# Performance work log

Hardware: AMD Instinct MI355X
Metric: run time of the kernel (lower is better)

Reference implementation:

```python
import jax, jax.numpy as jnp
import numpy as np
import math

MAX_REL_POS = 32  # max_relative_position

def _sincos_table(d_model, max_len):
    pos = np.arange(max_len)[:, None].astype(np.float32)
    div = np.exp(np.arange(0, d_model, 2).astype(np.float32) * (-math.log(10000.0) / d_model))
    pe = np.zeros((max_len, d_model), dtype=np.float32)
    pe[:, 0::2] = np.sin(pos * div)
    pe[:, 1::2] = np.cos(pos * div)
    return jnp.asarray(pe)

def setup_inputs() -> dict:
    rng = jax.random.key(0)
    k1, k2, k3 = jax.random.split(rng, 3)
    B, H, S, D = 4, 16, 1024, 64
    pe = _sincos_table(D, 2 * MAX_REL_POS + 1)  # fixed (non-trainable) buffer
    return {
        "query": jax.random.normal(k1, (B, H, S, D), jnp.float32),
        "key": jax.random.normal(k2, (B, H, S, D), jnp.float32),
        "value": jax.random.normal(k3, (B, H, S, D), jnp.float32),
        "pe_k": pe,
        "pe_v": pe,
    }

def reference(query, key, value, pe_k, pe_v):
    B, H, S, D = query.shape
    # relative distance indices: clip(k - q, -P, P) + P  -> [S, S]
    dist = jnp.clip(jnp.arange(S)[None, :] - jnp.arange(S)[:, None],
                    -MAX_REL_POS, MAX_REL_POS) + MAX_REL_POS
    R_k = pe_k[dist]  # [S, S, D]
    R_v = pe_v[dist]  # [S, S, D]
    scores = jnp.einsum('bhqd,bhkd->bhqk', query, key)
    scores = scores + jnp.einsum('bhqd,qkd->bhqk', query, R_k)
    scores = scores / math.sqrt(D)
    # one_direction=True -> causal mask
    causal = jnp.tril(jnp.ones((S, S), dtype=bool))
    scores = jnp.where(causal[None, None], scores, jnp.float32(-1e9))
    p_attn = jax.nn.softmax(scores, axis=-1)
    output = jnp.einsum('bhqk,bhkd->bhqd', p_attn, value)
    output = output + jnp.einsum('bhqv,qvd->bhqd', p_attn, R_v)
    return output, p_attn
```

## Files before the change

kernel.cpp:

```cpp
#include <hip/hip_runtime.h>

typedef __attribute__((ext_vector_type(8))) short bfrag;
typedef __attribute__((ext_vector_type(4))) float ffrag;

namespace {
constexpr int Sc = 1024, Dc = 64;
constexpr int P2 = 72;
constexpr float SCALE = 0.125f;
}

__device__ __forceinline__ unsigned short f2bf(float f) {
    unsigned u = __builtin_bit_cast(unsigned, f);
    u += 0x7fffu + ((u >> 16) & 1u);
    return (unsigned short)(u >> 16);
}
__device__ __forceinline__ bfrag pack8(float4 a, float4 b) {
    bfrag r;
    r[0] = (short)f2bf(a.x); r[1] = (short)f2bf(a.y);
    r[2] = (short)f2bf(a.z); r[3] = (short)f2bf(a.w);
    r[4] = (short)f2bf(b.x); r[5] = (short)f2bf(b.y);
    r[6] = (short)f2bf(b.z); r[7] = (short)f2bf(b.w);
    return r;
}
#define MFMA(a, b, c) __builtin_amdgcn_mfma_f32_16x16x32_bf16((a), (b), (c), 0, 0, 0)

__global__ __launch_bounds__(256, 3)
void relattn(const float* __restrict__ Qg, const float* __restrict__ Kg,
             const float* __restrict__ Vg, const float* __restrict__ pek,
             const float* __restrict__ pev, float* __restrict__ outg,
             float* __restrict__ pbuf)
{
    __shared__ __align__(16) char smem[53760];
    unsigned short* Qs = (unsigned short*)smem;
    unsigned short* Ks = (unsigned short*)(smem + 9216);
    unsigned short* Vt = (unsigned short*)(smem + 18432);
    unsigned short* Pt = (unsigned short*)(smem + 27648);
    float* Ts = (float*)(smem + 36864);
    float* Ws = (float*)(smem + 45312);
    float* W0 = (float*)(smem + 53504);
    float* Ot = (float*)(smem + 9216);

    const int tid  = threadIdx.x;
    const int bh   = blockIdx.y;
    const int wv   = tid >> 6;
    const int lane = tid & 63;
    const int n    = lane & 15;
    const int quad = lane >> 4;

    const float* Qbh = Qg + (size_t)bh * Sc * Dc;
    const float* Kbh = Kg + (size_t)bh * Sc * Dc;
    const float* Vbh = Vg + (size_t)bh * Sc * Dc;
    float* pbh = pbuf + (size_t)bh * Sc * Sc;
    float* obh = outg + (size_t)bh * Sc * Dc;

    const int sr  = tid >> 2;
    const int sc  = (tid & 3) * 16;
    const int kp  = tid & 31;
    const int vd0 = (tid >> 5) * 8;

    for (int half = 0; half < 2; ++half) {
        const int qt = half ? (15 - (int)blockIdx.x) : (int)blockIdx.x;
        const int qrow = wv * 16 + quad * 4;

        __syncthreads();

        {
            const float* src = Qbh + (size_t)(qt * 64 + sr) * Dc + sc;
            float4 a = *(const float4*)(src);
            float4 b = *(const float4*)(src + 4);
            float4 c = *(const float4*)(src + 8);
            float4 d = *(const float4*)(src + 12);
            *(bfrag*)&Qs[sr * P2 + sc]     = pack8(a, b);
            *(bfrag*)&Qs[sr * P2 + sc + 8] = pack8(c, d);
        }
        for (int idx = tid; idx < 64 * 32; idx += 256) Ws[idx] = 0.f;
        for (int i = tid; i < 135; i += 256) {
            bfrag z = {};
            *(bfrag*)&Ks[33 * P2 + i * 8] = z;
        }
        if (tid < 132) {
            int r = tid >> 2, c0 = (tid & 3) * 16;
            const float* src = pek + (size_t)r * Dc + c0;
            float4 a = *(const float4*)(src);
            float4 b = *(const float4*)(src + 4);
            float4 c = *(const float4*)(src + 8);
            float4 d = *(const float4*)(src + 12);
            *(bfrag*)&Ks[r * P2 + c0]     = pack8(a, b);
            *(bfrag*)&Ks[r * P2 + c0 + 8] = pack8(c, d);
        }
        __syncthreads();

        bfrag qa0 = *(bfrag*)&Qs[(wv * 16 + n) * P2 + quad * 8];
        bfrag qa1 = *(bfrag*)&Qs[(wv * 16 + n) * P2 + 32 + quad * 8];

        #pragma unroll
        for (int sub = 0; sub < 3; ++sub) {
            bfrag b0 = *(bfrag*)&Ks[(sub * 16 + n) * P2 + quad * 8];
            bfrag b1 = *(bfrag*)&Ks[(sub * 16 + n) * P2 + 32 + quad * 8];
            ffrag c = {};
            c = MFMA(qa0, b0, c);
            c = MFMA(qa1, b1, c);
            int j = sub * 16 + n;
            if (j <= 32) {
                #pragma unroll
                for (int reg = 0; reg < 4; ++reg)
                    Ts[(qrow + reg) * 33 + j] = c[reg];
            }
        }
        __syncthreads();

        float ts0[4];
        #pragma unroll
        for (int reg = 0; reg < 4; ++reg) ts0[reg] = Ts[(qrow + reg) * 33];

        {
            const int zb = (qt + 1) * 64;
            if (zb < Sc) {
                const int z4 = (Sc - zb) >> 2;
                const float4 z = make_float4(0.f, 0.f, 0.f, 0.f);
                for (int r = 0; r < 64; ++r) {
                    float4* rp = (float4*)(pbh + (size_t)(qt * 64 + r) * Sc + zb);
                    for (int c4 = tid; c4 < z4; c4 += 256) rp[c4] = z;
                }
            }
        }

        float lsum[4] = {0.f, 0.f, 0.f, 0.f};
        for (int kt = 0; kt <= qt; ++kt) {
            const bool bnd = (kt >= qt - 1);
            const float* ksrc = Kbh + (size_t)(kt * 64 + sr) * Dc + sc;
            float4 ka = *(const float4*)(ksrc);
            float4 kb = *(const float4*)(ksrc + 4);
            float4 kc = *(const float4*)(ksrc + 8);
            float4 kd = *(const float4*)(ksrc + 12);
            __syncthreads();
            *(bfrag*)&Ks[sr * P2 + sc]     = pack8(ka, kb);
            *(bfrag*)&Ks[sr * P2 + sc + 8] = pack8(kc, kd);
            __syncthreads();
            #pragma unroll
            for (int sub = 0; sub < 4; ++sub) {
                bfrag b0 = *(bfrag*)&Ks[(sub * 16 + n) * P2 + quad * 8];
                bfrag b1 = *(bfrag*)&Ks[(sub * 16 + n) * P2 + 32 + quad * 8];
                ffrag c = {};
                c = MFMA(qa0, b0, c);
                c = MFMA(qa1, b1, c);
                const int k = kt * 64 + sub * 16 + n;
                if (!bnd) {
                    #pragma unroll
                    for (int reg = 0; reg < 4; ++reg)
                        lsum[reg] += __expf((c[reg] + ts0[reg]) * SCALE);
                } else {
                    #pragma unroll
                    for (int reg = 0; reg < 4; ++reg) {
                        int jrel = k - (qt * 64 + qrow + reg) + 32;
                        if (jrel <= 32) {
                            int jcl = jrel < 0 ? 0 : jrel;
                            lsum[reg] += __expf((c[reg] + Ts[(qrow + reg) * 33 + jcl]) * SCALE);
                        }
                    }
                }
            }
        }
        float rinv[4];
        #pragma unroll
        for (int reg = 0; reg < 4; ++reg) {
            float l = lsum[reg];
            l += __shfl_xor(l, 1);
            l += __shfl_xor(l, 2);
            l += __shfl_xor(l, 4);
            l += __shfl_xor(l, 8);
            rinv[reg] = 1.f / l;
        }

        ffrag oacc[4];
        #pragma unroll
        for (int i = 0; i < 4; ++i) { ffrag z = {}; oacc[i] = z; }

        for (int kt = 0; kt <= qt; ++kt) {
            const bool bnd = (kt >= qt - 1);
            const float* ksrc = Kbh + (size_t)(kt * 64 + sr) * Dc + sc;
            float4 ka = *(const float4*)(ksrc);
            float4 kb = *(const float4*)(ksrc + 4);
            float4 kc = *(const float4*)(ksrc + 8);
            float4 kd = *(const float4*)(ksrc + 12);
            const float* vsrc = Vbh + (size_t)(kt * 64 + 2 * kp) * Dc + vd0;
            float4 v0a = *(const float4*)(vsrc);
            float4 v0b = *(const float4*)(vsrc + 4);
            float4 v1a = *(const float4*)(vsrc + Dc);
            float4 v1b = *(const float4*)(vsrc + Dc + 4);
            __syncthreads();
            *(bfrag*)&Ks[sr * P2 + sc]     = pack8(ka, kb);
            *(bfrag*)&Ks[sr * P2 + sc + 8] = pack8(kc, kd);
            {
                float r0[8] = {v0a.x, v0a.y, v0a.z, v0a.w, v0b.x, v0b.y, v0b.z, v0b.w};
                float r1[8] = {v1a.x, v1a.y, v1a.z, v1a.w, v1b.x, v1b.y, v1b.z, v1b.w};
                #pragma unroll
                for (int i = 0; i < 8; ++i) {
                    unsigned pk = (unsigned)f2bf(r0[i]) | ((unsigned)f2bf(r1[i]) << 16);
                    *(unsigned*)&Vt[(vd0 + i) * P2 + 2 * kp] = pk;
                }
            }
            __syncthreads();
            #pragma unroll
            for (int sub = 0; sub < 4; ++sub) {
                bfrag b0 = *(bfrag*)&Ks[(sub * 16 + n) * P2 + quad * 8];
                bfrag b1 = *(bfrag*)&Ks[(sub * 16 + n) * P2 + 32 + quad * 8];
                ffrag c = {};
                c = MFMA(qa0, b0, c);
                c = MFMA(qa1, b1, c);
                const int k = kt * 64 + sub * 16 + n;
                float* prow = pbh + (size_t)(qt * 64 + qrow) * Sc + k;
                if (!bnd) {
                    #pragma unroll
                    for (int reg = 0; reg < 4; ++reg) {
                        float p = __expf((c[reg] + ts0[reg]) * SCALE) * rinv[reg];
                        prow[(size_t)reg * Sc] = p;
                        Pt[(qrow + reg) * P2 + sub * 16 + n] = (unsigned short)f2bf(p);
                    }
                } else {
                    #pragma unroll
                    for (int reg = 0; reg < 4; ++reg) {
                        int jrel = k - (qt * 64 + qrow + reg) + 32;
                        float p = 0.f;
                        if (jrel <= 32) {
                            int jcl = jrel < 0 ? 0 : jrel;
                            p = __expf((c[reg] + Ts[(qrow + reg) * 33 + jcl]) * SCALE) * rinv[reg];
                        }
                        prow[(size_t)reg * Sc] = p;
                        Pt[(qrow + reg) * P2 + sub * 16 + n] = (unsigned short)f2bf(p);
                        if ((unsigned)(jrel - 1) < 32u) Ws[(qrow + reg) * 32 + jrel - 1] = p;
                    }
                }
            }
            __syncthreads();
            bfrag pb0 = *(bfrag*)&Pt[(wv * 16 + n) * P2 + quad * 8];
            bfrag pb1 = *(bfrag*)&Pt[(wv * 16 + n) * P2 + 32 + quad * 8];
            #pragma unroll
            for (int ds = 0; ds < 4; ++ds) {
                bfrag va0 = *(bfrag*)&Vt[(ds * 16 + n) * P2 + quad * 8];
                bfrag va1 = *(bfrag*)&Vt[(ds * 16 + n) * P2 + 32 + quad * 8];
                oacc[ds] = MFMA(va0, pb0, oacc[ds]);
                oacc[ds] = MFMA(va1, pb1, oacc[ds]);
            }
        }

        __syncthreads();
        if (tid < 64) {
            float s = 0.f;
            #pragma unroll
            for (int j = 0; j < 32; ++j) s += Ws[tid * 32 + j];
            W0[tid] = 1.f - s;
        }
        {
            int q = tid >> 2, j0 = (tid & 3) * 8;
            #pragma unroll
            for (int i = 0; i < 8; i += 2) {
                unsigned pk = (unsigned)f2bf(Ws[q * 32 + j0 + i]) |
                              ((unsigned)f2bf(Ws[q * 32 + j0 + i + 1]) << 16);
                *(unsigned*)&Pt[q * P2 + j0 + i] = pk;
            }
        }
        {
            int jj = tid >> 3, d0 = (tid & 7) * 8;
            const float* src = pev + (size_t)(jj + 1) * Dc + d0;
            float4 a = *(const float4*)(src);
            float4 b = *(const float4*)(src + 4);
            float vr[8] = {a.x, a.y, a.z, a.w, b.x, b.y, b.z, b.w};
            #pragma unroll
            for (int i = 0; i < 8; ++i)
                Vt[(d0 + i) * P2 + jj] = (unsigned short)f2bf(vr[i]);
        }
        __syncthreads();
        {
            bfrag pb = *(bfrag*)&Pt[(wv * 16 + n) * P2 + quad * 8];
            #pragma unroll
            for (int ds = 0; ds < 4; ++ds) {
                bfrag va = *(bfrag*)&Vt[(ds * 16 + n) * P2 + quad * 8];
                oacc[ds] = MFMA(va, pb, oacc[ds]);
            }
        }
        float w0q = W0[wv * 16 + n];
        __syncthreads();
        #pragma unroll
        for (int ds = 0; ds < 4; ++ds) {
            float4 ov;
            ov.x = oacc[ds][0] + w0q * pev[ds * 16 + quad * 4 + 0];
            ov.y = oacc[ds][1] + w0q * pev[ds * 16 + quad * 4 + 1];
            ov.z = oacc[ds][2] + w0q * pev[ds * 16 + quad * 4 + 2];
            ov.w = oacc[ds][3] + w0q * pev[ds * 16 + quad * 4 + 3];
            *(float4*)&Ot[(wv * 16 + n) * 68 + ds * 16 + quad * 4] = ov;
        }
        __syncthreads();
        {
            int r = tid >> 2, c0 = (tid & 3) * 16;
            float* dst = obh + (size_t)(qt * 64 + r) * Dc + c0;
            *(float4*)(dst)      = *(float4*)&Ot[r * 68 + c0];
            *(float4*)(dst + 4)  = *(float4*)&Ot[r * 68 + c0 + 4];
            *(float4*)(dst + 8)  = *(float4*)&Ot[r * 68 + c0 + 8];
            *(float4*)(dst + 12) = *(float4*)&Ot[r * 68 + c0 + 12];
        }
    }
}

extern "C" void kernel_launch(void* const* d_in, const int* in_sizes, int n_in,
                              void* d_out, int out_size, void* d_ws, size_t ws_size,
                              hipStream_t stream)
{
    const float* Q   = (const float*)d_in[0];
    const float* K   = (const float*)d_in[1];
    const float* V   = (const float*)d_in[2];
    const float* pek = (const float*)d_in[3];
    const float* pev = (const float*)d_in[4];
    float* out  = (float*)d_out;
    float* pbuf = out + (size_t)64 * Sc * Dc;

    dim3 grid(8, 64);
    relattn<<<grid, 256, 0, stream>>>(Q, K, V, pek, pev, out, pbuf);
}
```

Measured before the change: 391.3 us.

## Fuse two-pass softmax into a single pass with double-buffered K/V prefetch

Drops the separate row-sum pass over K. Unnormalized probabilities are written to the P output and fed to the PV MFMA in one sweep, and the 1/sum scaling is applied afterwards to the output accumulator and in a rescale pass over the written P rows. K and V tiles now use double-buffered LDS: the next tile's global loads are issued before the current tile's compute, which removes one sync pair per iteration. Shared memory grows to about 72 KB and the occupancy hint drops from 3 to 2 blocks. The P matrix is read back and rewritten once for normalization, and exp is applied without subtracting a running max.

```diff
diff --git a/kernel.cpp b/kernel.cpp
--- a/kernel.cpp
+++ b/kernel.cpp
@@ -24,20 +24,23 @@
 }
 #define MFMA(a, b, c) __builtin_amdgcn_mfma_f32_16x16x32_bf16((a), (b), (c), 0, 0, 0)
 
-__global__ __launch_bounds__(256, 3)
+__global__ __launch_bounds__(256, 2)
 void relattn(const float* __restrict__ Qg, const float* __restrict__ Kg,
              const float* __restrict__ Vg, const float* __restrict__ pek,
              const float* __restrict__ pev, float* __restrict__ outg,
              float* __restrict__ pbuf)
 {
-    __shared__ __align__(16) char smem[53760];
-    unsigned short* Qs = (unsigned short*)smem;
-    unsigned short* Ks = (unsigned short*)(smem + 9216);
-    unsigned short* Vt = (unsigned short*)(smem + 18432);
-    unsigned short* Pt = (unsigned short*)(smem + 27648);
-    float* Ts = (float*)(smem + 36864);
-    float* Ws = (float*)(smem + 45312);
-    float* W0 = (float*)(smem + 53504);
+    __shared__ __align__(16) char smem[72448];
+    unsigned short* Qs  = (unsigned short*)smem;
+    unsigned short* Ks0 = (unsigned short*)(smem + 9216);
+    unsigned short* Ks1 = (unsigned short*)(smem + 18432);
+    unsigned short* Vt0 = (unsigned short*)(smem + 27648);
+    unsigned short* Vt1 = (unsigned short*)(smem + 36864);
+    unsigned short* Pt  = (unsigned short*)(smem + 46080);
+    float* Ts = (float*)(smem + 55296);
+    float* Ws = (float*)(smem + 63744);
+    float* W0 = (float*)(smem + 71936);
+    float* Rl = (float*)(smem + 72192);
     float* Ot = (float*)(smem + 9216);
 
     const int tid  = threadIdx.x;
@@ -76,7 +79,7 @@
         for (int idx = tid; idx < 64 * 32; idx += 256) Ws[idx] = 0.f;
         for (int i = tid; i < 135; i += 256) {
             bfrag z = {};
-            *(bfrag*)&Ks[33 * P2 + i * 8] = z;
+            *(bfrag*)&Ks0[33 * P2 + i * 8] = z;
         }
         if (tid < 132) {
             int r = tid >> 2, c0 = (tid & 3) * 16;
@@ -85,8 +88,21 @@
             float4 b = *(const float4*)(src + 4);
             float4 c = *(const float4*)(src + 8);
             float4 d = *(const float4*)(src + 12);
-            *(bfrag*)&Ks[r * P2 + c0]     = pack8(a, b);
-            *(bfrag*)&Ks[r * P2 + c0 + 8] = pack8(c, d);
+            *(bfrag*)&Ks0[r * P2 + c0]     = pack8(a, b);
+            *(bfrag*)&Ks0[r * P2 + c0 + 8] = pack8(c, d);
+        }
+        float4 ka, kb, kc, kd, v0a, v0b, v1a, v1b;
+        {
+            const float* ksrc = Kbh + (size_t)sr * Dc + sc;
+            ka = *(const float4*)(ksrc);
+            kb = *(const float4*)(ksrc + 4);
+            kc = *(const float4*)(ksrc + 8);
+            kd = *(const float4*)(ksrc + 12);
+            const float* vsrc = Vbh + (size_t)(2 * kp) * Dc + vd0;
+            v0a = *(const float4*)(vsrc);
+            v0b = *(const float4*)(vsrc + 4);
+            v1a = *(const float4*)(vsrc + Dc);
+            v1b = *(const float4*)(vsrc + Dc + 4);
         }
         __syncthreads();
 
@@ -95,8 +111,8 @@
 
         #pragma unroll
         for (int sub = 0; sub < 3; ++sub) {
-            bfrag b0 = *(bfrag*)&Ks[(sub * 16 + n) * P2 + quad * 8];
-            bfrag b1 = *(bfrag*)&Ks[(sub * 16 + n) * P2 + 32 + quad * 8];
+            bfrag b0 = *(bfrag*)&Ks0[(sub * 16 + n) * P2 + quad * 8];
+            bfrag b1 = *(bfrag*)&Ks0[(sub * 16 + n) * P2 + 32 + quad * 8];
             ffrag c = {};
             c = MFMA(qa0, b0, c);
             c = MFMA(qa1, b1, c);
@@ -113,98 +129,50 @@
         #pragma unroll
         for (int reg = 0; reg < 4; ++reg) ts0[reg] = Ts[(qrow + reg) * 33];
 
-        {
-            const int zb = (qt + 1) * 64;
-            if (zb < Sc) {
-                const int z4 = (Sc - zb) >> 2;
-                const float4 z = make_float4(0.f, 0.f, 0.f, 0.f);
-                for (int r = 0; r < 64; ++r) {
-                    float4* rp = (float4*)(pbh + (size_t)(qt * 64 + r) * Sc + zb);
-                    for (int c4 = tid; c4 < z4; c4 += 256) rp[c4] = z;
-                }
-            }
-        }
+        *(bfrag*)&Ks0[sr * P2 + sc]     = pack8(ka, kb);
+        *(bfrag*)&Ks0[sr * P2 + sc + 8] = pack8(kc, kd);
+        {
+            float r0[8] = {v0a.x, v0a.y, v0a.z, v0a.w, v0b.x, v0b.y, v0b.z, v0b.w};
+            float r1[8] = {v1a.x, v1a.y, v1a.z, v1a.w, v1b.x, v1b.y, v1b.z, v1b.w};
+            #pragma unroll
+            for (int i = 0; i < 8; ++i) {
+                unsigned pk = (unsigned)f2bf(r0[i]) | ((unsigned)f2bf(r1[i]) << 16);
+                *(unsigned*)&Vt0[(vd0 + i) * P2 + 2 * kp] = pk;
+            }
+        }
+        __syncthreads();
 
         float lsum[4] = {0.f, 0.f, 0.f, 0.f};
+        ffrag oacc[4];
+        #pragma unroll
+        for (int i = 0; i < 4; ++i) { ffrag z = {}; oacc[i] = z; }
+
         for (int kt = 0; kt <= qt; ++kt) {
             const bool bnd = (kt >= qt - 1);
-            const float* ksrc = Kbh + (size_t)(kt * 64 + sr) * Dc + sc;
-            float4 ka = *(const float4*)(ksrc);
-            float4 kb = *(const float4*)(ksrc + 4);
-            float4 kc = *(const float4*)(ksrc + 8);
-            float4 kd = *(const float4*)(ksrc + 12);
-            __syncthreads();
-            *(bfrag*)&Ks[sr * P2 + sc]     = pack8(ka, kb);
-            *(bfrag*)&Ks[sr * P2 + sc + 8] = pack8(kc, kd);
-            __syncthreads();
+            const bool pf  = (kt < qt);
+            unsigned short* Kc = (kt & 1) ? Ks1 : Ks0;
+            unsigned short* Vc = (kt & 1) ? Vt1 : Vt0;
+            unsigned short* Kn = (kt & 1) ? Ks0 : Ks1;
+            unsigned short* Vn = (kt & 1) ? Vt0 : Vt1;
+
+            float4 nka, nkb, nkc, nkd, nv0a, nv0b, nv1a, nv1b;
+            if (pf) {
+                const float* ksrc = Kbh + (size_t)((kt + 1) * 64 + sr) * Dc + sc;
+                nka = *(const float4*)(ksrc);
+                nkb = *(const float4*)(ksrc + 4);
+                nkc = *(const float4*)(ksrc + 8);
+                nkd = *(const float4*)(ksrc + 12);
+                const float* vsrc = Vbh + (size_t)((kt + 1) * 64 + 2 * kp) * Dc + vd0;
+                nv0a = *(const float4*)(vsrc);
+                nv0b = *(const float4*)(vsrc + 4);
+                nv1a = *(const float4*)(vsrc + Dc);
+                nv1b = *(const float4*)(vsrc + Dc + 4);
+            }
+
             #pragma unroll
             for (int sub = 0; sub < 4; ++sub) {
-                bfrag b0 = *(bfrag*)&Ks[(sub * 16 + n) * P2 + quad * 8];
-                bfrag b1 = *(bfrag*)&Ks[(sub * 16 + n) * P2 + 32 + quad * 8];
-                ffrag c = {};
-                c = MFMA(qa0, b0, c);
-                c = MFMA(qa1, b1, c);
-                const int k = kt * 64 + sub * 16 + n;
-                if (!bnd) {
-                    #pragma unroll
-                    for (int reg = 0; reg < 4; ++reg)
-                        lsum[reg] += __expf((c[reg] + ts0[reg]) * SCALE);
-                } else {
-                    #pragma unroll
-                    for (int reg = 0; reg < 4; ++reg) {
-                        int jrel = k - (qt * 64 + qrow + reg) + 32;
-                        if (jrel <= 32) {
-                            int jcl = jrel < 0 ? 0 : jrel;
-                            lsum[reg] += __expf((c[reg] + Ts[(qrow + reg) * 33 + jcl]) * SCALE);
-                        }
-                    }
-                }
-            }
-        }
-        float rinv[4];
-        #pragma unroll
-        for (int reg = 0; reg < 4; ++reg) {
-            float l = lsum[reg];
-            l += __shfl_xor(l, 1);
-            l += __shfl_xor(l, 2);
-            l += __shfl_xor(l, 4);
-            l += __shfl_xor(l, 8);
-            rinv[reg] = 1.f / l;
-        }
-
-        ffrag oacc[4];
-        #pragma unroll
-        for (int i = 0; i < 4; ++i) { ffrag z = {}; oacc[i] = z; }
-
-        for (int kt = 0; kt <= qt; ++kt) {
-            const bool bnd = (kt >= qt - 1);
-            const float* ksrc = Kbh + (size_t)(kt * 64 + sr) * Dc + sc;
-            float4 ka = *(const float4*)(ksrc);
-            float4 kb = *(const float4*)(ksrc + 4);
-            float4 kc = *(const float4*)(ksrc + 8);
-            float4 kd = *(const float4*)(ksrc + 12);
-            const float* vsrc = Vbh + (size_t)(kt * 64 + 2 * kp) * Dc + vd0;
-            float4 v0a = *(const float4*)(vsrc);
-            float4 v0b = *(const float4*)(vsrc + 4);
-            float4 v1a = *(const float4*)(vsrc + Dc);
-            float4 v1b = *(const float4*)(vsrc + Dc + 4);
-            __syncthreads();
-            *(bfrag*)&Ks[sr * P2 + sc]     = pack8(ka, kb);
-            *(bfrag*)&Ks[sr * P2 + sc + 8] = pack8(kc, kd);
-            {
-                float r0[8] = {v0a.x, v0a.y, v0a.z, v0a.w, v0b.x, v0b.y, v0b.z, v0b.w};
-                float r1[8] = {v1a.x, v1a.y, v1a.z, v1a.w, v1b.x, v1b.y, v1b.z, v1b.w};
-                #pragma unroll
-                for (int i = 0; i < 8; ++i) {
-                    unsigned pk = (unsigned)f2bf(r0[i]) | ((unsigned)f2bf(r1[i]) << 16);
-                    *(unsigned*)&Vt[(vd0 + i) * P2 + 2 * kp] = pk;
-                }
-            }
-            __syncthreads();
-            #pragma unroll
-            for (int sub = 0; sub < 4; ++sub) {
-                bfrag b0 = *(bfrag*)&Ks[(sub * 16 + n) * P2 + quad * 8];
-                bfrag b1 = *(bfrag*)&Ks[(sub * 16 + n) * P2 + 32 + quad * 8];
+                bfrag b0 = *(bfrag*)&Kc[(sub * 16 + n) * P2 + quad * 8];
+                bfrag b1 = *(bfrag*)&Kc[(sub * 16 + n) * P2 + 32 + quad * 8];
                 ffrag c = {};
                 c = MFMA(qa0, b0, c);
                 c = MFMA(qa1, b1, c);
@@ -213,7 +181,8 @@
                 if (!bnd) {
                     #pragma unroll
                     for (int reg = 0; reg < 4; ++reg) {
-                        float p = __expf((c[reg] + ts0[reg]) * SCALE) * rinv[reg];
+                        float p = __expf((c[reg] + ts0[reg]) * SCALE);
+                        lsum[reg] += p;
                         prow[(size_t)reg * Sc] = p;
                         Pt[(qrow + reg) * P2 + sub * 16 + n] = (unsigned short)f2bf(p);
                     }
@@ -224,7 +193,8 @@
                         float p = 0.f;
                         if (jrel <= 32) {
                             int jcl = jrel < 0 ? 0 : jrel;
-                            p = __expf((c[reg] + Ts[(qrow + reg) * 33 + jcl]) * SCALE) * rinv[reg];
+                            p = __expf((c[reg] + Ts[(qrow + reg) * 33 + jcl]) * SCALE);
+                            lsum[reg] += p;
                         }
                         prow[(size_t)reg * Sc] = p;
                         Pt[(qrow + reg) * P2 + sub * 16 + n] = (unsigned short)f2bf(p);
@@ -232,24 +202,52 @@
                     }
                 }
             }
+            if (pf) {
+                *(bfrag*)&Kn[sr * P2 + sc]     = pack8(nka, nkb);
+                *(bfrag*)&Kn[sr * P2 + sc + 8] = pack8(nkc, nkd);
+                float r0[8] = {nv0a.x, nv0a.y, nv0a.z, nv0a.w, nv0b.x, nv0b.y, nv0b.z, nv0b.w};
+                float r1[8] = {nv1a.x, nv1a.y, nv1a.z, nv1a.w, nv1b.x, nv1b.y, nv1b.z, nv1b.w};
+                #pragma unroll
+                for (int i = 0; i < 8; ++i) {
+                    unsigned pk = (unsigned)f2bf(r0[i]) | ((unsigned)f2bf(r1[i]) << 16);
+                    *(unsigned*)&Vn[(vd0 + i) * P2 + 2 * kp] = pk;
+                }
+            }
             __syncthreads();
+
             bfrag pb0 = *(bfrag*)&Pt[(wv * 16 + n) * P2 + quad * 8];
             bfrag pb1 = *(bfrag*)&Pt[(wv * 16 + n) * P2 + 32 + quad * 8];
             #pragma unroll
             for (int ds = 0; ds < 4; ++ds) {
-                bfrag va0 = *(bfrag*)&Vt[(ds * 16 + n) * P2 + quad * 8];
-                bfrag va1 = *(bfrag*)&Vt[(ds * 16 + n) * P2 + 32 + quad * 8];
+                bfrag va0 = *(bfrag*)&Vc[(ds * 16 + n) * P2 + quad * 8];
+                bfrag va1 = *(bfrag*)&Vc[(ds * 16 + n) * P2 + 32 + quad * 8];
                 oacc[ds] = MFMA(va0, pb0, oacc[ds]);
                 oacc[ds] = MFMA(va1, pb1, oacc[ds]);
             }
-        }
-
-        __syncthreads();
+            __syncthreads();
+        }
+
+        float rinv[4];
+        #pragma unroll
+        for (int reg = 0; reg < 4; ++reg) {
+            float l = lsum[reg];
+            l += __shfl_xor(l, 1);
+            l += __shfl_xor(l, 2);
+            l += __shfl_xor(l, 4);
+            l += __shfl_xor(l, 8);
+            rinv[reg] = 1.f / l;
+        }
+        if (n == 0) {
+            #pragma unroll
+            for (int reg = 0; reg < 4; ++reg) Rl[qrow + reg] = rinv[reg];
+        }
+        __syncthreads();
+
         if (tid < 64) {
             float s = 0.f;
             #pragma unroll
             for (int j = 0; j < 32; ++j) s += Ws[tid * 32 + j];
-            W0[tid] = 1.f - s;
+            W0[tid] = 1.f - Rl[tid] * s;
         }
         {
             int q = tid >> 2, j0 = (tid & 3) * 8;
@@ -268,26 +266,47 @@
             float vr[8] = {a.x, a.y, a.z, a.w, b.x, b.y, b.z, b.w};
             #pragma unroll
             for (int i = 0; i < 8; ++i)
-                Vt[(d0 + i) * P2 + jj] = (unsigned short)f2bf(vr[i]);
-        }
-        __syncthreads();
+                Vt0[(d0 + i) * P2 + jj] = (unsigned short)f2bf(vr[i]);
+        }
+
+        {
+            const int n4 = (qt + 1) * 16;
+            float* const base = pbh + (size_t)(qt * 64) * Sc;
+            if (tid < n4) {
+                #pragma unroll 4
+                for (int r = 0; r < 64; ++r) {
+                    float4* rp = (float4*)(base + (size_t)r * Sc) + tid;
+                    float4 v = *rp;
+                    float s = Rl[r];
+                    v.x *= s; v.y *= s; v.z *= s; v.w *= s;
+                    *rp = v;
+                }
+            } else {
+                const float4 z = make_float4(0.f, 0.f, 0.f, 0.f);
+                #pragma unroll 8
+                for (int r = 0; r < 64; ++r)
+                    *((float4*)(base + (size_t)r * Sc) + tid) = z;
+            }
+        }
+        __syncthreads();
+
         {
             bfrag pb = *(bfrag*)&Pt[(wv * 16 + n) * P2 + quad * 8];
             #pragma unroll
             for (int ds = 0; ds < 4; ++ds) {
-                bfrag va = *(bfrag*)&Vt[(ds * 16 + n) * P2 + quad * 8];
+                bfrag va = *(bfrag*)&Vt0[(ds * 16 + n) * P2 + quad * 8];
                 oacc[ds] = MFMA(va, pb, oacc[ds]);
             }
         }
         float w0q = W0[wv * 16 + n];
-        __syncthreads();
+        float rq  = Rl[wv * 16 + n];
         #pragma unroll
         for (int ds = 0; ds < 4; ++ds) {
             float4 ov;
-            ov.x = oacc[ds][0] + w0q * pev[ds * 16 + quad * 4 + 0];
-            ov.y = oacc[ds][1] + w0q * pev[ds * 16 + quad * 4 + 1];
-            ov.z = oacc[ds][2] + w0q * pev[ds * 16 + quad * 4 + 2];
-            ov.w = oacc[ds][3] + w0q * pev[ds * 16 + quad * 4 + 3];
+            ov.x = oacc[ds][0] * rq + w0q * pev[ds * 16 + quad * 4 + 0];
+            ov.y = oacc[ds][1] * rq + w0q * pev[ds * 16 + quad * 4 + 1];
+            ov.z = oacc[ds][2] * rq + w0q * pev[ds * 16 + quad * 4 + 2];
+            ov.w = oacc[ds][3] * rq + w0q * pev[ds * 16 + quad * 4 + 3];
             *(float4*)&Ot[(wv * 16 + n) * 68 + ds * 16 + quad * 4] = ov;
         }
         __syncthreads();
```

Result: slower. 444.2 us (+13.5%).

## Double-buffer K tiles and prefetch K/V into registers across iterations

Applied to the files above, without the earlier changes.

Adds a second K shared-memory buffer and software-prefetches the next K and V tiles into registers, so global loads overlap the MFMA and exp work of the current tile. This removes one of the two barriers per iteration in both the row-sum and output passes. Ws gets a padded stride of 33 to reduce LDS bank conflicts, and Q moves to an aliased region. The cost is higher register pressure at 3 blocks per CU and more complex aliasing of shared memory (Qs/Ws, Ot/Ks0), which could introduce hazards.

```diff
diff --git a/kernel.cpp b/kernel.cpp
--- a/kernel.cpp
+++ b/kernel.cpp
@@ -6,6 +6,8 @@
 namespace {
 constexpr int Sc = 1024, Dc = 64;
 constexpr int P2 = 72;
+constexpr int PQ = 64;
+constexpr int PW = 33;
 constexpr float SCALE = 0.125f;
 }
 
@@ -30,15 +32,16 @@
              const float* __restrict__ pev, float* __restrict__ outg,
              float* __restrict__ pbuf)
 {
-    __shared__ __align__(16) char smem[53760];
-    unsigned short* Qs = (unsigned short*)smem;
-    unsigned short* Ks = (unsigned short*)(smem + 9216);
-    unsigned short* Vt = (unsigned short*)(smem + 18432);
-    unsigned short* Pt = (unsigned short*)(smem + 27648);
+    __shared__ __align__(16) char smem[54016];
+    unsigned short* Ks0 = (unsigned short*)smem;
+    unsigned short* Ks1 = (unsigned short*)(smem + 9216);
+    unsigned short* Vt  = (unsigned short*)(smem + 18432);
+    unsigned short* Pt  = (unsigned short*)(smem + 27648);
     float* Ts = (float*)(smem + 36864);
+    unsigned short* Qs = (unsigned short*)(smem + 45312);
     float* Ws = (float*)(smem + 45312);
-    float* W0 = (float*)(smem + 53504);
-    float* Ot = (float*)(smem + 9216);
+    float* W0 = (float*)(smem + 53760);
+    float* Ot = (float*)smem;
 
     const int tid  = threadIdx.x;
     const int bh   = blockIdx.y;
@@ -54,7 +57,7 @@
     float* obh = outg + (size_t)bh * Sc * Dc;
 
     const int sr  = tid >> 2;
-    const int sc  = (tid & 3) * 16;
+    const int sc4 = (tid & 3) * 16;
     const int kp  = tid & 31;
     const int vd0 = (tid >> 5) * 8;
 
@@ -64,19 +67,26 @@
 
         __syncthreads();
 
-        {
-            const float* src = Qbh + (size_t)(qt * 64 + sr) * Dc + sc;
+        float4 k0a, k0b, k0c, k0d;
+        {
+            const float* ksrc = Kbh + (size_t)sr * Dc + sc4;
+            k0a = *(const float4*)(ksrc);
+            k0b = *(const float4*)(ksrc + 4);
+            k0c = *(const float4*)(ksrc + 8);
+            k0d = *(const float4*)(ksrc + 12);
+        }
+        {
+            const float* src = Qbh + (size_t)(qt * 64 + sr) * Dc + sc4;
             float4 a = *(const float4*)(src);
             float4 b = *(const float4*)(src + 4);
             float4 c = *(const float4*)(src + 8);
             float4 d = *(const float4*)(src + 12);
-            *(bfrag*)&Qs[sr * P2 + sc]     = pack8(a, b);
-            *(bfrag*)&Qs[sr * P2 + sc + 8] = pack8(c, d);
-        }
-        for (int idx = tid; idx < 64 * 32; idx += 256) Ws[idx] = 0.f;
+            *(bfrag*)&Qs[sr * PQ + sc4]     = pack8(a, b);
+            *(bfrag*)&Qs[sr * PQ + sc4 + 8] = pack8(c, d);
+        }
         for (int i = tid; i < 135; i += 256) {
             bfrag z = {};
-            *(bfrag*)&Ks[33 * P2 + i * 8] = z;
+            *(bfrag*)&Ks0[33 * P2 + i * 8] = z;
         }
         if (tid < 132) {
             int r = tid >> 2, c0 = (tid & 3) * 16;
@@ -85,18 +95,18 @@
             float4 b = *(const float4*)(src + 4);
             float4 c = *(const float4*)(src + 8);
             float4 d = *(const float4*)(src + 12);
-            *(bfrag*)&Ks[r * P2 + c0]     = pack8(a, b);
-            *(bfrag*)&Ks[r * P2 + c0 + 8] = pack8(c, d);
-        }
-        __syncthreads();
-
-        bfrag qa0 = *(bfrag*)&Qs[(wv * 16 + n) * P2 + quad * 8];
-        bfrag qa1 = *(bfrag*)&Qs[(wv * 16 + n) * P2 + 32 + quad * 8];
+            *(bfrag*)&Ks0[r * P2 + c0]     = pack8(a, b);
+            *(bfrag*)&Ks0[r * P2 + c0 + 8] = pack8(c, d);
+        }
+        __syncthreads();
+
+        bfrag qa0 = *(bfrag*)&Qs[(wv * 16 + n) * PQ + quad * 8];
+        bfrag qa1 = *(bfrag*)&Qs[(wv * 16 + n) * PQ + 32 + quad * 8];
 
         #pragma unroll
         for (int sub = 0; sub < 3; ++sub) {
-            bfrag b0 = *(bfrag*)&Ks[(sub * 16 + n) * P2 + quad * 8];
-            bfrag b1 = *(bfrag*)&Ks[(sub * 16 + n) * P2 + 32 + quad * 8];
+            bfrag b0 = *(bfrag*)&Ks0[(sub * 16 + n) * P2 + quad * 8];
+            bfrag b1 = *(bfrag*)&Ks0[(sub * 16 + n) * P2 + 32 + quad * 8];
             ffrag c = {};
             c = MFMA(qa0, b0, c);
             c = MFMA(qa1, b1, c);
@@ -104,14 +114,26 @@
             if (j <= 32) {
                 #pragma unroll
                 for (int reg = 0; reg < 4; ++reg)
-                    Ts[(qrow + reg) * 33 + j] = c[reg];
-            }
+                    Ts[(qrow + reg) * PW + j] = c[reg];
+            }
+        }
+        *(bfrag*)&Ks1[sr * P2 + sc4]     = pack8(k0a, k0b);
+        *(bfrag*)&Ks1[sr * P2 + sc4 + 8] = pack8(k0c, k0d);
+        float4 pka, pkb, pkc, pkd;
+        if (qt >= 1) {
+            const float* ksrc = Kbh + (size_t)(64 + sr) * Dc + sc4;
+            pka = *(const float4*)(ksrc);
+            pkb = *(const float4*)(ksrc + 4);
+            pkc = *(const float4*)(ksrc + 8);
+            pkd = *(const float4*)(ksrc + 12);
         }
         __syncthreads();
 
         float ts0[4];
         #pragma unroll
-        for (int reg = 0; reg < 4; ++reg) ts0[reg] = Ts[(qrow + reg) * 33];
+        for (int reg = 0; reg < 4; ++reg) ts0[reg] = Ts[(qrow + reg) * PW];
+
+        for (int idx = tid; idx < 64 * PW; idx += 256) Ws[idx] = 0.f;
 
         {
             const int zb = (qt + 1) * 64;
@@ -128,19 +150,12 @@
         float lsum[4] = {0.f, 0.f, 0.f, 0.f};
         for (int kt = 0; kt <= qt; ++kt) {
             const bool bnd = (kt >= qt - 1);
-            const float* ksrc = Kbh + (size_t)(kt * 64 + sr) * Dc + sc;
-            float4 ka = *(const float4*)(ksrc);
-            float4 kb = *(const float4*)(ksrc + 4);
-            float4 kc = *(const float4*)(ksrc + 8);
-            float4 kd = *(const float4*)(ksrc + 12);
-            __syncthreads();
-            *(bfrag*)&Ks[sr * P2 + sc]     = pack8(ka, kb);
-            *(bfrag*)&Ks[sr * P2 + sc + 8] = pack8(kc, kd);
-            __syncthreads();
+            unsigned short* Kc = (kt & 1) ? Ks0 : Ks1;
+            unsigned short* Kn = (kt & 1) ? Ks1 : Ks0;
             #pragma unroll
             for (int sub = 0; sub < 4; ++sub) {
-                bfrag b0 = *(bfrag*)&Ks[(sub * 16 + n) * P2 + quad * 8];
-                bfrag b1 = *(bfrag*)&Ks[(sub * 16 + n) * P2 + 32 + quad * 8];
+                bfrag b0 = *(bfrag*)&Kc[(sub * 16 + n) * P2 + quad * 8];
+                bfrag b1 = *(bfrag*)&Kc[(sub * 16 + n) * P2 + 32 + quad * 8];
                 ffrag c = {};
                 c = MFMA(qa0, b0, c);
                 c = MFMA(qa1, b1, c);
@@ -155,11 +170,23 @@
                         int jrel = k - (qt * 64 + qrow + reg) + 32;
                         if (jrel <= 32) {
                             int jcl = jrel < 0 ? 0 : jrel;
-                            lsum[reg] += __expf((c[reg] + Ts[(qrow + reg) * 33 + jcl]) * SCALE);
+                            lsum[reg] += __expf((c[reg] + Ts[(qrow + reg) * PW + jcl]) * SCALE);
                         }
                     }
                 }
             }
+            if (kt < qt) {
+                *(bfrag*)&Kn[sr * P2 + sc4]     = pack8(pka, pkb);
+                *(bfrag*)&Kn[sr * P2 + sc4 + 8] = pack8(pkc, pkd);
+            }
+            if (kt + 2 <= qt) {
+                const float* ksrc = Kbh + (size_t)((kt + 2) * 64 + sr) * Dc + sc4;
+                pka = *(const float4*)(ksrc);
+                pkb = *(const float4*)(ksrc + 4);
+                pkc = *(const float4*)(ksrc + 8);
+                pkd = *(const float4*)(ksrc + 12);
+            }
+            __syncthreads();
         }
         float rinv[4];
         #pragma unroll
@@ -172,39 +199,45 @@
             rinv[reg] = 1.f / l;
         }
 
+        {
+            const float* ksrc = Kbh + (size_t)sr * Dc + sc4;
+            float4 a = *(const float4*)(ksrc);
+            float4 b = *(const float4*)(ksrc + 4);
+            float4 c = *(const float4*)(ksrc + 8);
+            float4 d = *(const float4*)(ksrc + 12);
+            *(bfrag*)&Ks0[sr * P2 + sc4]     = pack8(a, b);
+            *(bfrag*)&Ks0[sr * P2 + sc4 + 8] = pack8(c, d);
+        }
+        if (qt >= 1) {
+            const float* ksrc = Kbh + (size_t)(64 + sr) * Dc + sc4;
+            pka = *(const float4*)(ksrc);
+            pkb = *(const float4*)(ksrc + 4);
+            pkc = *(const float4*)(ksrc + 8);
+            pkd = *(const float4*)(ksrc + 12);
+        }
+        float4 pva, pvb, pvc, pvd;
+        {
+            const float* vsrc = Vbh + (size_t)(2 * kp) * Dc + vd0;
+            pva = *(const float4*)(vsrc);
+            pvb = *(const float4*)(vsrc + 4);
+            pvc = *(const float4*)(vsrc + Dc);
+            pvd = *(const float4*)(vsrc + Dc + 4);
+        }
+        __syncthreads();
+
         ffrag oacc[4];
         #pragma unroll
         for (int i = 0; i < 4; ++i) { ffrag z = {}; oacc[i] = z; }
 
         for (int kt = 0; kt <= qt; ++kt) {
             const bool bnd = (kt >= qt - 1);
-            const float* ksrc = Kbh + (size_t)(kt * 64 + sr) * Dc + sc;
-            float4 ka = *(const float4*)(ksrc);
-            float4 kb = *(const float4*)(ksrc + 4);
-            float4 kc = *(const float4*)(ksrc + 8);
-            float4 kd = *(const float4*)(ksrc + 12);
-            const float* vsrc = Vbh + (size_t)(kt * 64 + 2 * kp) * Dc + vd0;
-            float4 v0a = *(const float4*)(vsrc);
-            float4 v0b = *(const float4*)(vsrc + 4);
-            float4 v1a = *(const float4*)(vsrc + Dc);
-            float4 v1b = *(const float4*)(vsrc + Dc + 4);
-            __syncthreads();
-            *(bfrag*)&Ks[sr * P2 + sc]     = pack8(ka, kb);
-            *(bfrag*)&Ks[sr * P2 + sc + 8] = pack8(kc, kd);
-            {
-                float r0[8] = {v0a.x, v0a.y, v0a.z, v0a.w, v0b.x, v0b.y, v0b.z, v0b.w};
-                float r1[8] = {v1a.x, v1a.y, v1a.z, v1a.w, v1b.x, v1b.y, v1b.z, v1b.w};
-                #pragma unroll
-                for (int i = 0; i < 8; ++i) {
-                    unsigned pk = (unsigned)f2bf(r0[i]) | ((unsigned)f2bf(r1[i]) << 16);
-                    *(unsigned*)&Vt[(vd0 + i) * P2 + 2 * kp] = pk;
-                }
-            }
-            __syncthreads();
+            unsigned short* Kc = (kt & 1) ? Ks1 : Ks0;
+            unsigned short* Kn = (kt & 1) ? Ks0 : Ks1;
+
             #pragma unroll
             for (int sub = 0; sub < 4; ++sub) {
-                bfrag b0 = *(bfrag*)&Ks[(sub * 16 + n) * P2 + quad * 8];
-                bfrag b1 = *(bfrag*)&Ks[(sub * 16 + n) * P2 + 32 + quad * 8];
+                bfrag b0 = *(bfrag*)&Kc[(sub * 16 + n) * P2 + quad * 8];
+                bfrag b1 = *(bfrag*)&Kc[(sub * 16 + n) * P2 + 32 + quad * 8];
                 ffrag c = {};
                 c = MFMA(qa0, b0, c);
                 c = MFMA(qa1, b1, c);
@@ -224,13 +257,40 @@
                         float p = 0.f;
                         if (jrel <= 32) {
                             int jcl = jrel < 0 ? 0 : jrel;
-                            p = __expf((c[reg] + Ts[(qrow + reg) * 33 + jcl]) * SCALE) * rinv[reg];
+                            p = __expf((c[reg] + Ts[(qrow + reg) * PW + jcl]) * SCALE) * rinv[reg];
                         }
                         prow[(size_t)reg * Sc] = p;
                         Pt[(qrow + reg) * P2 + sub * 16 + n] = (unsigned short)f2bf(p);
-                        if ((unsigned)(jrel - 1) < 32u) Ws[(qrow + reg) * 32 + jrel - 1] = p;
+                        if ((unsigned)(jrel - 1) < 32u) Ws[(qrow + reg) * PW + jrel - 1] = p;
                     }
                 }
+            }
+            if (kt < qt) {
+                *(bfrag*)&Kn[sr * P2 + sc4]     = pack8(pka, pkb);
+                *(bfrag*)&Kn[sr * P2 + sc4 + 8] = pack8(pkc, pkd);
+            }
+            {
+                float r0[8] = {pva.x, pva.y, pva.z, pva.w, pvb.x, pvb.y, pvb.z, pvb.w};
+                float r1[8] = {pvc.x, pvc.y, pvc.z, pvc.w, pvd.x, pvd.y, pvd.z, pvd.w};
+                #pragma unroll
+                for (int i = 0; i < 8; ++i) {
+                    unsigned pk = (unsigned)f2bf(r0[i]) | ((unsigned)f2bf(r1[i]) << 16);
+                    *(unsigned*)&Vt[(vd0 + i) * P2 + 2 * kp] = pk;
+                }
+            }
+            if (kt + 2 <= qt) {
+                const float* ksrc = Kbh + (size_t)((kt + 2) * 64 + sr) * Dc + sc4;
+                pka = *(const float4*)(ksrc);
+                pkb = *(const float4*)(ksrc + 4);
+                pkc = *(const float4*)(ksrc + 8);
+                pkd = *(const float4*)(ksrc + 12);
+            }
+            if (kt < qt) {
+                const float* vsrc = Vbh + (size_t)((kt + 1) * 64 + 2 * kp) * Dc + vd0;
+                pva = *(const float4*)(vsrc);
+                pvb = *(const float4*)(vsrc + 4);
+                pvc = *(const float4*)(vsrc + Dc);
+                pvd = *(const float4*)(vsrc + Dc + 4);
             }
             __syncthreads();
             bfrag pb0 = *(bfrag*)&Pt[(wv * 16 + n) * P2 + quad * 8];
@@ -242,21 +302,21 @@
                 oacc[ds] = MFMA(va0, pb0, oacc[ds]);
                 oacc[ds] = MFMA(va1, pb1, oacc[ds]);
             }
-        }
-
-        __syncthreads();
+            __syncthreads();
+        }
+
         if (tid < 64) {
             float s = 0.f;
             #pragma unroll
-            for (int j = 0; j < 32; ++j) s += Ws[tid * 32 + j];
+            for (int j = 0; j < 32; ++j) s += Ws[tid * PW + j];
             W0[tid] = 1.f - s;
         }
         {
             int q = tid >> 2, j0 = (tid & 3) * 8;
             #pragma unroll
             for (int i = 0; i < 8; i += 2) {
-                unsigned pk = (unsigned)f2bf(Ws[q * 32 + j0 + i]) |
-                              ((unsigned)f2bf(Ws[q * 32 + j0 + i + 1]) << 16);
+                unsigned pk = (unsigned)f2bf(Ws[q * PW + j0 + i]) |
+                              ((unsigned)f2bf(Ws[q * PW + j0 + i + 1]) << 16);
                 *(unsigned*)&Pt[q * P2 + j0 + i] = pk;
             }
         }
@@ -280,7 +340,6 @@
             }
         }
         float w0q = W0[wv * 16 + n];
-        __syncthreads();
         #pragma unroll
         for (int ds = 0; ds < 4; ++ds) {
             float4 ov;
```

Result: no change. 392.0 us (+0.2%).
